# Kernel optimization log

Measured on AMD Instinct MI355X. Metric: run time of the kernel, lower is better.

The kernel has to match this reference:

```python
import jax, jax.numpy as jnp
import numpy as np

B, T, N, D, H = 16, 12, 325, 64, 4
E = 2600
NEG_SLOPE = 0.2
LN_EPS = 1e-5
SM_EPS = 1e-16


def setup_inputs() -> dict:
    key = jax.random.key(0)
    ks = jax.random.split(key, 8)
    x = jax.random.normal(ks[0], (B, T, N, D), dtype=jnp.float32)
    edge_index = jax.random.randint(ks[1], (2, E), 0, N, dtype=jnp.int64)
    W = jax.random.normal(ks[2], (D, H, D), dtype=jnp.float32) * 0.05   # lin weight, [in, heads, out]
    att_src = jax.random.normal(ks[3], (H, D), dtype=jnp.float32) * 0.05
    att_dst = jax.random.normal(ks[4], (H, D), dtype=jnp.float32) * 0.05
    bias = jnp.zeros((D,), dtype=jnp.float32)
    gamma = jnp.ones((D,), dtype=jnp.float32)
    beta = jnp.zeros((D,), dtype=jnp.float32)
    return {"x": x, "W": W, "att_src": att_src, "att_dst": att_dst,
            "bias": bias, "gamma": gamma, "beta": beta, "edge_index": edge_index}


def reference(x, W, att_src, att_dst, bias, gamma, beta, edge_index):
    b, t, n, d = x.shape
    bt = b * t
    xb = x.reshape(bt, n, d)

    # add self-loops (GATConv default add_self_loops=True)
    loops = jnp.arange(n, dtype=edge_index.dtype)
    src = jnp.concatenate([edge_index[0], loops])  # message source j
    dst = jnp.concatenate([edge_index[1], loops])  # message target i

    # per-head linear projection, node axis leading for segment ops: [N, BT, H, D]
    xp = jnp.einsum('bnd,dhf->nbhf', xb, W)

    a_src = jnp.einsum('nbhf,hf->nbh', xp, att_src)  # [N, BT, H]
    a_dst = jnp.einsum('nbhf,hf->nbh', xp, att_dst)

    alpha = a_src[src] + a_dst[dst]                  # [Etot, BT, H]
    alpha = jnp.where(alpha >= 0, alpha, NEG_SLOPE * alpha)

    # segment softmax over incoming edges of each dst node
    m = jax.ops.segment_max(alpha, dst, num_segments=n)        # [N, BT, H]
    e = jnp.exp(alpha - m[dst])
    s = jax.ops.segment_sum(e, dst, num_segments=n)            # [N, BT, H]
    coef = e / (s[dst] + SM_EPS)                               # [Etot, BT, H]

    # weighted scatter-sum aggregation
    msgs = coef[..., None] * xp[src]                           # [Etot, BT, H, D]
    out = jax.ops.segment_sum(msgs, dst, num_segments=n)       # [N, BT, H, D]

    out = out.mean(axis=2) + bias                              # concat=False -> head mean; [N, BT, D]
    out = out.transpose(1, 0, 2).reshape(b, t, n, d)

    # residual + LayerNorm
    y = x + out
    mu = y.mean(axis=-1, keepdims=True)
    var = y.var(axis=-1, keepdims=True)
    return (y - mu) * jax.lax.rsqrt(var + LN_EPS) * gamma + beta
```

## Files before the change

kernel.cpp:

```cpp
#include <hip/hip_runtime.h>

#define Nn 325
#define Dd 64
#define Hh 4
#define Ee 2600
#define BT 192
#define ETOT (Ee+Nn)
#define NROWS (BT*Nn)
#define XPS 136

#define XP_B   (Nn * XPS * 2)
#define COEF_B (ETOT * 8)
#define SMEM_BYTES (XP_B + COEF_B + 2600 + 2600 + ((Nn + 1) * 4) + (ETOT * 4))

typedef __attribute__((ext_vector_type(8))) short bf16x8;
typedef __attribute__((ext_vector_type(4))) float f32x4;

static __device__ __forceinline__ short f2bf(float f) {
    union { float f; unsigned u; } v; v.f = f;
    unsigned r = v.u + 0x7fffu + ((v.u >> 16) & 1u);
    return (short)(r >> 16);
}
static __device__ __forceinline__ float bf_lo(unsigned p) {
    union { unsigned u; float f; } v; v.u = p << 16; return v.f;
}
static __device__ __forceinline__ float bf_hi(unsigned p) {
    union { unsigned u; float f; } v; v.u = p & 0xffff0000u; return v.f;
}

__global__ __launch_bounds__(256) void k_pre(
    const float* __restrict__ W, unsigned short* __restrict__ Wt,
    const int* __restrict__ ei, int* __restrict__ offs, int* __restrict__ elist)
{
    const int t = threadIdx.x;
    if (blockIdx.x < 64) {
        const int f = blockIdx.x * 256 + t;
        const int thr = f >> 6, idx = f & 63;
        const int ct = idx >> 4, kk = (idx >> 3) & 1, j = idx & 7;
        const int w = thr >> 6, lane = thr & 63;
        const int q = lane >> 4, l16 = lane & 15;
        Wt[f] = (unsigned short)f2bf(
            W[(size_t)(kk * 32 + q * 8 + j) * 256 + w * 64 + ct * 16 + l16]);
        return;
    }
    __shared__ int cnt[Nn + 1];
    __shared__ int cur[Nn];
    const int lane = t & 63;
    for (int i = t; i <= Nn; i += 256) cnt[i] = 0;
    __syncthreads();
    for (int e = t; e < ETOT; e += 256) {
        int d = (e < Ee) ? ei[Ee + e] : (e - Ee);
        atomicAdd(&cnt[d + 1], 1);
    }
    __syncthreads();
    if (t < 64) {
        int run = 0;
        for (int c = 0; c < 6; ++c) {
            int i = c * 64 + lane;
            int v = (i <= Nn) ? cnt[i] : 0;
            #pragma unroll
            for (int off = 1; off < 64; off <<= 1) {
                int u = __shfl_up(v, off);
                if (lane >= off) v += u;
            }
            v += run;
            if (i <= Nn) cnt[i] = v;
            run = __shfl(v, 63);
        }
    }
    __syncthreads();
    for (int i = t; i <= Nn; i += 256) offs[i] = cnt[i];
    for (int i = t; i < Nn; i += 256) cur[i] = cnt[i];
    __syncthreads();
    for (int e = t; e < ETOT; e += 256) {
        int s, d;
        if (e < Ee) { s = ei[e]; d = ei[Ee + e]; }
        else        { s = e - Ee; d = e - Ee; }
        int slot = atomicAdd(&cur[d], 1);
        elist[slot] = s;
    }
}

__global__ __launch_bounds__(1024, 4) void k_fused(
    const float* __restrict__ x, const unsigned short* __restrict__ Wt,
    const float* __restrict__ att_src, const float* __restrict__ att_dst,
    const int* __restrict__ offs, const int* __restrict__ elist,
    const float* __restrict__ bias, const float* __restrict__ gamma,
    const float* __restrict__ beta, float* __restrict__ out)
{
    const int bt   = blockIdx.x;
    const int t    = threadIdx.x;
    const int wv   = t >> 6;
    const int lane = t & 63;
    const int q    = lane >> 4;
    const int l16  = lane & 15;
    const int btN  = bt * Nn;

    extern __shared__ char smem[];
    unsigned short* xpS   = (unsigned short*)smem;
    float2*         coefS = (float2*)(smem + XP_B);
    float*          asrcS = (float*)(smem + XP_B + COEF_B);
    float*          adstS = asrcS + 2 * Nn;
    int*            offsS = (int*)(adstS + 2 * Nn);
    int*            elistS= offsS + (Nn + 1);

    for (int i = t; i < ETOT; i += 1024) elistS[i] = elist[i];
    for (int i = t; i <= Nn; i += 1024) offsS[i] = offs[i];

    float accO[6][4];
    #pragma unroll
    for (int i = 0; i < 6; ++i)
        accO[i][0] = accO[i][1] = accO[i][2] = accO[i][3] = 0.f;

    const int hh  = wv >> 3;
    const int rtb = wv & 7;

    #pragma unroll 2
    for (int p = 0; p < 2; ++p) {
        const int h = p * 2 + hh;
        bf16x8 bfr[4][2];
        const bf16x8* wtp = (const bf16x8*)(Wt + (size_t)(h * 64 + lane) * 64);
        #pragma unroll
        for (int ct = 0; ct < 4; ++ct) {
            bfr[ct][0] = wtp[ct * 2];
            bfr[ct][1] = wtp[ct * 2 + 1];
        }
        float avs[4], avd[4];
        #pragma unroll
        for (int ct = 0; ct < 4; ++ct) {
            avs[ct] = att_src[h * 64 + ct * 16 + l16];
            avd[ct] = att_dst[h * 64 + ct * 16 + l16];
        }
        if (p) __syncthreads();

        #pragma unroll
        for (int k3 = 0; k3 < 3; ++k3) {
            const int rt = rtb + 8 * k3;
            if (rt > 20) break;
            bf16x8 afr[2];
            const int na = min(rt * 16 + l16, Nn - 1);
            const float* xr = x + (size_t)(btN + na) * 64 + q * 8;
            #pragma unroll
            for (int kk = 0; kk < 2; ++kk) {
                float4 v0 = *(const float4*)(xr + kk * 32);
                float4 v1 = *(const float4*)(xr + kk * 32 + 4);
                afr[kk][0]=f2bf(v0.x); afr[kk][1]=f2bf(v0.y);
                afr[kk][2]=f2bf(v0.z); afr[kk][3]=f2bf(v0.w);
                afr[kk][4]=f2bf(v1.x); afr[kk][5]=f2bf(v1.y);
                afr[kk][6]=f2bf(v1.z); afr[kk][7]=f2bf(v1.w);
            }
            f32x4 acc[4];
            #pragma unroll
            for (int ct = 0; ct < 4; ++ct) {
                acc[ct] = (f32x4){0.f, 0.f, 0.f, 0.f};
                acc[ct] = __builtin_amdgcn_mfma_f32_16x16x32_bf16(afr[0], bfr[ct][0], acc[ct], 0, 0, 0);
                acc[ct] = __builtin_amdgcn_mfma_f32_16x16x32_bf16(afr[1], bfr[ct][1], acc[ct], 0, 0, 0);
            }
            #pragma unroll
            for (int r = 0; r < 4; ++r) {
                const int n = rt * 16 + q * 4 + r;
                float ps = 0.f, pd = 0.f;
                #pragma unroll
                for (int ct = 0; ct < 4; ++ct) {
                    ps = fmaf(acc[ct][r], avs[ct], ps);
                    pd = fmaf(acc[ct][r], avd[ct], pd);
                }
                #pragma unroll
                for (int off = 1; off <= 8; off <<= 1) {
                    ps += __shfl_xor(ps, off);
                    pd += __shfl_xor(pd, off);
                }
                if (l16 == 0 && n < Nn) {
                    asrcS[n * 2 + hh] = ps;
                    adstS[n * 2 + hh] = pd;
                }
                if (n < Nn) {
                    #pragma unroll
                    for (int ct = 0; ct < 4; ++ct)
                        xpS[n * XPS + (ct * 16 + l16) * 2 + hh] =
                            (unsigned short)f2bf(acc[ct][r]);
                }
            }
        }
        __syncthreads();

        #pragma unroll
        for (int it = 0; it < 6; ++it) {
            const int n = wv * 4 + q + it * 64;
            if (n >= Nn) break;
            const int o0 = offsS[n];
            int deg = offsS[n + 1] - o0;
            deg = min(deg, 48);
            const float adn0 = adstS[n * 2], adn1 = adstS[n * 2 + 1];
            float ex0[3], ex1[3];
            float m0 = -3e38f, m1 = -3e38f;
            #pragma unroll
            for (int r = 0; r < 3; ++r) {
                float a0 = -3e38f, a1 = -3e38f;
                if (r * 16 < deg) {
                    const int e = r * 16 + l16;
                    if (e < deg) {
                        const int j = elistS[o0 + e];
                        const float2 as = *(const float2*)(asrcS + j * 2);
                        a0 = as.x + adn0; a1 = as.y + adn1;
                    }
                }
                a0 = (a0 >= 0.f) ? a0 : 0.2f * a0;
                a1 = (a1 >= 0.f) ? a1 : 0.2f * a1;
                ex0[r] = a0; ex1[r] = a1;
                m0 = fmaxf(m0, a0); m1 = fmaxf(m1, a1);
            }
            #pragma unroll
            for (int off = 1; off <= 8; off <<= 1) {
                m0 = fmaxf(m0, __shfl_xor(m0, off));
                m1 = fmaxf(m1, __shfl_xor(m1, off));
            }
            float s0 = 0.f, s1 = 0.f;
            #pragma unroll
            for (int r = 0; r < 3; ++r) if (r * 16 < deg) {
                ex0[r] = __expf(ex0[r] - m0); s0 += ex0[r];
                ex1[r] = __expf(ex1[r] - m1); s1 += ex1[r];
            }
            #pragma unroll
            for (int off = 1; off <= 8; off <<= 1) {
                s0 += __shfl_xor(s0, off);
                s1 += __shfl_xor(s1, off);
            }
            const float i0 = 1.f / (s0 + 1e-16f);
            const float i1 = 1.f / (s1 + 1e-16f);
            #pragma unroll
            for (int r = 0; r < 3; ++r) if (r * 16 < deg) {
                const int e = r * 16 + l16;
                if (e < deg) coefS[o0 + e] = make_float2(ex0[r] * i0, ex1[r] * i1);
            }

            float f0 = 0.f, f1 = 0.f, f2v = 0.f, f3 = 0.f;
            int e2 = 0;
            for (; e2 + 2 <= deg; e2 += 2) {
                const int ja = elistS[o0 + e2];
                const int jb = elistS[o0 + e2 + 1];
                const float2 ca = coefS[o0 + e2];
                const float2 cb = coefS[o0 + e2 + 1];
                const uint4 ra = *(const uint4*)((const char*)xpS + ja * (XPS * 2) + l16 * 16);
                const uint4 rb = *(const uint4*)((const char*)xpS + jb * (XPS * 2) + l16 * 16);
                f0  = fmaf(ca.x, bf_lo(ra.x), f0);  f0  = fmaf(ca.y, bf_hi(ra.x), f0);
                f1  = fmaf(ca.x, bf_lo(ra.y), f1);  f1  = fmaf(ca.y, bf_hi(ra.y), f1);
                f2v = fmaf(ca.x, bf_lo(ra.z), f2v); f2v = fmaf(ca.y, bf_hi(ra.z), f2v);
                f3  = fmaf(ca.x, bf_lo(ra.w), f3);  f3  = fmaf(ca.y, bf_hi(ra.w), f3);
                f0  = fmaf(cb.x, bf_lo(rb.x), f0);  f0  = fmaf(cb.y, bf_hi(rb.x), f0);
                f1  = fmaf(cb.x, bf_lo(rb.y), f1);  f1  = fmaf(cb.y, bf_hi(rb.y), f1);
                f2v = fmaf(cb.x, bf_lo(rb.z), f2v); f2v = fmaf(cb.y, bf_hi(rb.z), f2v);
                f3  = fmaf(cb.x, bf_lo(rb.w), f3);  f3  = fmaf(cb.y, bf_hi(rb.w), f3);
            }
            if (e2 < deg) {
                const int ja = elistS[o0 + e2];
                const float2 ca = coefS[o0 + e2];
                const uint4 ra = *(const uint4*)((const char*)xpS + ja * (XPS * 2) + l16 * 16);
                f0  = fmaf(ca.x, bf_lo(ra.x), f0);  f0  = fmaf(ca.y, bf_hi(ra.x), f0);
                f1  = fmaf(ca.x, bf_lo(ra.y), f1);  f1  = fmaf(ca.y, bf_hi(ra.y), f1);
                f2v = fmaf(ca.x, bf_lo(ra.z), f2v); f2v = fmaf(ca.y, bf_hi(ra.z), f2v);
                f3  = fmaf(ca.x, bf_lo(ra.w), f3);  f3  = fmaf(ca.y, bf_hi(ra.w), f3);
            }
            accO[it][0] += f0; accO[it][1] += f1;
            accO[it][2] += f2v; accO[it][3] += f3;
        }
    }

    const int f4 = l16 * 4;
    const float4 ga = *(const float4*)(gamma + f4);
    const float4 be = *(const float4*)(beta + f4);
    const float4 bi = *(const float4*)(bias + f4);
    #pragma unroll
    for (int it = 0; it < 6; ++it) {
        const int n = wv * 4 + q + it * 64;
        if (n >= Nn) break;
        const float4 xv = *(const float4*)(x + (size_t)(btN + n) * 64 + f4);
        const float y0 = xv.x + accO[it][0] * 0.25f + bi.x;
        const float y1 = xv.y + accO[it][1] * 0.25f + bi.y;
        const float y2 = xv.z + accO[it][2] * 0.25f + bi.z;
        const float y3 = xv.w + accO[it][3] * 0.25f + bi.w;
        float s1 = y0 + y1 + y2 + y3;
        float s2 = y0*y0 + y1*y1 + y2*y2 + y3*y3;
        #pragma unroll
        for (int off = 1; off <= 8; off <<= 1) {
            s1 += __shfl_xor(s1, off);
            s2 += __shfl_xor(s2, off);
        }
        const float mu  = s1 * (1.f / 64.f);
        const float var = s2 * (1.f / 64.f) - mu * mu;
        const float rr  = rsqrtf(var + 1e-5f);
        float4 o;
        o.x = (y0 - mu) * rr * ga.x + be.x;
        o.y = (y1 - mu) * rr * ga.y + be.y;
        o.z = (y2 - mu) * rr * ga.z + be.z;
        o.w = (y3 - mu) * rr * ga.w + be.w;
        *(float4*)(out + (size_t)(btN + n) * 64 + f4) = o;
    }
}

extern "C" void kernel_launch(void* const* d_in, const int* in_sizes, int n_in,
                              void* d_out, int out_size, void* d_ws, size_t ws_size,
                              hipStream_t stream)
{
    const float* x       = (const float*)d_in[0];
    const float* W       = (const float*)d_in[1];
    const float* att_src = (const float*)d_in[2];
    const float* att_dst = (const float*)d_in[3];
    const float* bias    = (const float*)d_in[4];
    const float* gamma   = (const float*)d_in[5];
    const float* beta    = (const float*)d_in[6];
    const int*   ei      = (const int*)d_in[7];

    unsigned short* Wt = (unsigned short*)d_ws;
    int* offs  = (int*)(Wt + 16384);
    int* elist = offs + (Nn + 1);
    float* out = (float*)d_out;

    hipFuncSetAttribute((const void*)k_fused,
                        hipFuncAttributeMaxDynamicSharedMemorySize, SMEM_BYTES);

    hipLaunchKernelGGL(k_pre, dim3(65), dim3(256), 0, stream,
                       W, Wt, ei, offs, elist);
    hipLaunchKernelGGL(k_fused, dim3(BT), dim3(1024), SMEM_BYTES, stream,
                       x, Wt, att_src, att_dst, offs, elist,
                       bias, gamma, beta, out);
}
```

Before: 139.4 us.

## Pre-convert x to bf16, sort nodes by degree, unroll gather by four

Adds a pre-pass in k_pre that converts all of x to bf16 in workspace, so the fused kernel loads MFMA A fragments directly without per-element conversion. Builds a degree-sorted node permutation (descending degree histogram scan) so that each wave's four node groups have similar in-degree, which reduces divergence in the softmax and aggregation loops. The aggregation inner loop is unrolled to four edges for more LDS load-level parallelism. In exchange, the pre-pass writes and the fused kernel rereads an extra bf16 copy of x, and the output rows written per wave become scattered.

```diff
diff --git a/kernel.cpp b/kernel.cpp
--- a/kernel.cpp
+++ b/kernel.cpp
@@ -11,7 +11,7 @@
 
 #define XP_B   (Nn * XPS * 2)
 #define COEF_B (ETOT * 8)
-#define SMEM_BYTES (XP_B + COEF_B + 2600 + 2600 + ((Nn + 1) * 4) + (ETOT * 4))
+#define SMEM_BYTES (XP_B + COEF_B + 2600 + 2600 + ((Nn + 1) * 4) + (ETOT * 4) + (Nn * 4))
 
 typedef __attribute__((ext_vector_type(8))) short bf16x8;
 typedef __attribute__((ext_vector_type(4))) float f32x4;
@@ -30,7 +30,9 @@
 
 __global__ __launch_bounds__(256) void k_pre(
     const float* __restrict__ W, unsigned short* __restrict__ Wt,
-    const int* __restrict__ ei, int* __restrict__ offs, int* __restrict__ elist)
+    const int* __restrict__ ei, int* __restrict__ offs, int* __restrict__ elist,
+    int* __restrict__ perm, const float* __restrict__ x,
+    unsigned short* __restrict__ xbf)
 {
     const int t = threadIdx.x;
     if (blockIdx.x < 64) {
@@ -43,10 +45,30 @@
             W[(size_t)(kk * 32 + q * 8 + j) * 256 + w * 64 + ct * 16 + l16]);
         return;
     }
+    if (blockIdx.x >= 65) {
+        const int bx = blockIdx.x - 65;
+        #pragma unroll
+        for (int k = 0; k < 8; ++k) {
+            const int idx = bx * 2048 + k * 256 + t;
+            if (idx < (NROWS * Dd) / 4) {
+                float4 v = ((const float4*)x)[idx];
+                ushort4 o;
+                o.x = (unsigned short)f2bf(v.x);
+                o.y = (unsigned short)f2bf(v.y);
+                o.z = (unsigned short)f2bf(v.z);
+                o.w = (unsigned short)f2bf(v.w);
+                ((ushort4*)xbf)[idx] = o;
+            }
+        }
+        return;
+    }
     __shared__ int cnt[Nn + 1];
     __shared__ int cur[Nn];
+    __shared__ int dh[64];
+    __shared__ int startS[64];
     const int lane = t & 63;
     for (int i = t; i <= Nn; i += 256) cnt[i] = 0;
+    if (t < 64) dh[t] = 0;
     __syncthreads();
     for (int e = t; e < ETOT; e += 256) {
         int d = (e < Ee) ? ei[Ee + e] : (e - Ee);
@@ -71,6 +93,19 @@
     __syncthreads();
     for (int i = t; i <= Nn; i += 256) offs[i] = cnt[i];
     for (int i = t; i < Nn; i += 256) cur[i] = cnt[i];
+    for (int n = t; n < Nn; n += 256)
+        atomicAdd(&dh[min(cnt[n + 1] - cnt[n], 63)], 1);
+    __syncthreads();
+    if (t < 64) {
+        int v = dh[63 - lane];
+        int inc = v;
+        #pragma unroll
+        for (int off = 1; off < 64; off <<= 1) {
+            int u = __shfl_up(inc, off);
+            if (lane >= off) inc += u;
+        }
+        startS[63 - lane] = inc - v;
+    }
     __syncthreads();
     for (int e = t; e < ETOT; e += 256) {
         int s, d;
@@ -79,12 +114,18 @@
         int slot = atomicAdd(&cur[d], 1);
         elist[slot] = s;
     }
+    for (int n = t; n < Nn; n += 256) {
+        int slot = atomicAdd(&startS[min(cnt[n + 1] - cnt[n], 63)], 1);
+        perm[slot] = n;
+    }
 }
 
 __global__ __launch_bounds__(1024, 4) void k_fused(
-    const float* __restrict__ x, const unsigned short* __restrict__ Wt,
+    const float* __restrict__ x, const unsigned short* __restrict__ xbf,
+    const unsigned short* __restrict__ Wt,
     const float* __restrict__ att_src, const float* __restrict__ att_dst,
     const int* __restrict__ offs, const int* __restrict__ elist,
+    const int* __restrict__ perm,
     const float* __restrict__ bias, const float* __restrict__ gamma,
     const float* __restrict__ beta, float* __restrict__ out)
 {
@@ -103,9 +144,11 @@
     float*          adstS = asrcS + 2 * Nn;
     int*            offsS = (int*)(adstS + 2 * Nn);
     int*            elistS= offsS + (Nn + 1);
+    int*            permS = elistS + ETOT;
 
     for (int i = t; i < ETOT; i += 1024) elistS[i] = elist[i];
     for (int i = t; i <= Nn; i += 1024) offsS[i] = offs[i];
+    for (int i = t; i < Nn; i += 1024) permS[i] = perm[i];
 
     float accO[6][4];
     #pragma unroll
@@ -114,6 +157,7 @@
 
     const int hh  = wv >> 3;
     const int rtb = wv & 7;
+    const int g   = wv * 4 + q;
 
     #pragma unroll 2
     for (int p = 0; p < 2; ++p) {
@@ -137,18 +181,11 @@
         for (int k3 = 0; k3 < 3; ++k3) {
             const int rt = rtb + 8 * k3;
             if (rt > 20) break;
+            const int na = min(rt * 16 + l16, Nn - 1);
             bf16x8 afr[2];
-            const int na = min(rt * 16 + l16, Nn - 1);
-            const float* xr = x + (size_t)(btN + na) * 64 + q * 8;
-            #pragma unroll
-            for (int kk = 0; kk < 2; ++kk) {
-                float4 v0 = *(const float4*)(xr + kk * 32);
-                float4 v1 = *(const float4*)(xr + kk * 32 + 4);
-                afr[kk][0]=f2bf(v0.x); afr[kk][1]=f2bf(v0.y);
-                afr[kk][2]=f2bf(v0.z); afr[kk][3]=f2bf(v0.w);
-                afr[kk][4]=f2bf(v1.x); afr[kk][5]=f2bf(v1.y);
-                afr[kk][6]=f2bf(v1.z); afr[kk][7]=f2bf(v1.w);
-            }
+            #pragma unroll
+            for (int kk = 0; kk < 2; ++kk)
+                afr[kk] = *(const bf16x8*)(xbf + (size_t)(btN + na) * 64 + kk * 32 + q * 8);
             f32x4 acc[4];
             #pragma unroll
             for (int ct = 0; ct < 4; ++ct) {
@@ -186,8 +223,9 @@
 
         #pragma unroll
         for (int it = 0; it < 6; ++it) {
-            const int n = wv * 4 + q + it * 64;
-            if (n >= Nn) break;
+            const int rk = it * 64 + g;
+            if (rk >= Nn) continue;
+            const int n = permS[rk];
             const int o0 = offsS[n];
             int deg = offsS[n + 1] - o0;
             deg = min(deg, 48);
@@ -236,23 +274,33 @@
 
             float f0 = 0.f, f1 = 0.f, f2v = 0.f, f3 = 0.f;
             int e2 = 0;
-            for (; e2 + 2 <= deg; e2 += 2) {
-                const int ja = elistS[o0 + e2];
-                const int jb = elistS[o0 + e2 + 1];
-                const float2 ca = coefS[o0 + e2];
-                const float2 cb = coefS[o0 + e2 + 1];
-                const uint4 ra = *(const uint4*)((const char*)xpS + ja * (XPS * 2) + l16 * 16);
-                const uint4 rb = *(const uint4*)((const char*)xpS + jb * (XPS * 2) + l16 * 16);
-                f0  = fmaf(ca.x, bf_lo(ra.x), f0);  f0  = fmaf(ca.y, bf_hi(ra.x), f0);
-                f1  = fmaf(ca.x, bf_lo(ra.y), f1);  f1  = fmaf(ca.y, bf_hi(ra.y), f1);
-                f2v = fmaf(ca.x, bf_lo(ra.z), f2v); f2v = fmaf(ca.y, bf_hi(ra.z), f2v);
-                f3  = fmaf(ca.x, bf_lo(ra.w), f3);  f3  = fmaf(ca.y, bf_hi(ra.w), f3);
-                f0  = fmaf(cb.x, bf_lo(rb.x), f0);  f0  = fmaf(cb.y, bf_hi(rb.x), f0);
-                f1  = fmaf(cb.x, bf_lo(rb.y), f1);  f1  = fmaf(cb.y, bf_hi(rb.y), f1);
-                f2v = fmaf(cb.x, bf_lo(rb.z), f2v); f2v = fmaf(cb.y, bf_hi(rb.z), f2v);
-                f3  = fmaf(cb.x, bf_lo(rb.w), f3);  f3  = fmaf(cb.y, bf_hi(rb.w), f3);
-            }
-            if (e2 < deg) {
+            for (; e2 + 4 <= deg; e2 += 4) {
+                const int j0 = elistS[o0 + e2],     j1 = elistS[o0 + e2 + 1];
+                const int j2 = elistS[o0 + e2 + 2], j3 = elistS[o0 + e2 + 3];
+                const float2 c0 = coefS[o0 + e2],     c1 = coefS[o0 + e2 + 1];
+                const float2 c2 = coefS[o0 + e2 + 2], c3 = coefS[o0 + e2 + 3];
+                const uint4 r0 = *(const uint4*)((const char*)xpS + j0 * (XPS * 2) + l16 * 16);
+                const uint4 r1 = *(const uint4*)((const char*)xpS + j1 * (XPS * 2) + l16 * 16);
+                const uint4 r2 = *(const uint4*)((const char*)xpS + j2 * (XPS * 2) + l16 * 16);
+                const uint4 r3 = *(const uint4*)((const char*)xpS + j3 * (XPS * 2) + l16 * 16);
+                f0  = fmaf(c0.x, bf_lo(r0.x), f0);  f0  = fmaf(c0.y, bf_hi(r0.x), f0);
+                f1  = fmaf(c0.x, bf_lo(r0.y), f1);  f1  = fmaf(c0.y, bf_hi(r0.y), f1);
+                f2v = fmaf(c0.x, bf_lo(r0.z), f2v); f2v = fmaf(c0.y, bf_hi(r0.z), f2v);
+                f3  = fmaf(c0.x, bf_lo(r0.w), f3);  f3  = fmaf(c0.y, bf_hi(r0.w), f3);
+                f0  = fmaf(c1.x, bf_lo(r1.x), f0);  f0  = fmaf(c1.y, bf_hi(r1.x), f0);
+                f1  = fmaf(c1.x, bf_lo(r1.y), f1);  f1  = fmaf(c1.y, bf_hi(r1.y), f1);
+                f2v = fmaf(c1.x, bf_lo(r1.z), f2v); f2v = fmaf(c1.y, bf_hi(r1.z), f2v);
+                f3  = fmaf(c1.x, bf_lo(r1.w), f3);  f3  = fmaf(c1.y, bf_hi(r1.w), f3);
+                f0  = fmaf(c2.x, bf_lo(r2.x), f0);  f0  = fmaf(c2.y, bf_hi(r2.x), f0);
+                f1  = fmaf(c2.x, bf_lo(r2.y), f1);  f1  = fmaf(c2.y, bf_hi(r2.y), f1);
+                f2v = fmaf(c2.x, bf_lo(r2.z), f2v); f2v = fmaf(c2.y, bf_hi(r2.z), f2v);
+                f3  = fmaf(c2.x, bf_lo(r2.w), f3);  f3  = fmaf(c2.y, bf_hi(r2.w), f3);
+                f0  = fmaf(c3.x, bf_lo(r3.x), f0);  f0  = fmaf(c3.y, bf_hi(r3.x), f0);
+                f1  = fmaf(c3.x, bf_lo(r3.y), f1);  f1  = fmaf(c3.y, bf_hi(r3.y), f1);
+                f2v = fmaf(c3.x, bf_lo(r3.z), f2v); f2v = fmaf(c3.y, bf_hi(r3.z), f2v);
+                f3  = fmaf(c3.x, bf_lo(r3.w), f3);  f3  = fmaf(c3.y, bf_hi(r3.w), f3);
+            }
+            for (; e2 < deg; ++e2) {
                 const int ja = elistS[o0 + e2];
                 const float2 ca = coefS[o0 + e2];
                 const uint4 ra = *(const uint4*)((const char*)xpS + ja * (XPS * 2) + l16 * 16);
@@ -272,8 +320,9 @@
     const float4 bi = *(const float4*)(bias + f4);
     #pragma unroll
     for (int it = 0; it < 6; ++it) {
-        const int n = wv * 4 + q + it * 64;
-        if (n >= Nn) break;
+        const int rk = it * 64 + g;
+        if (rk >= Nn) continue;
+        const int n = permS[rk];
         const float4 xv = *(const float4*)(x + (size_t)(btN + n) * 64 + f4);
         const float y0 = xv.x + accO[it][0] * 0.25f + bi.x;
         const float y1 = xv.y + accO[it][1] * 0.25f + bi.y;
@@ -311,17 +360,19 @@
     const float* beta    = (const float*)d_in[6];
     const int*   ei      = (const int*)d_in[7];
 
-    unsigned short* Wt = (unsigned short*)d_ws;
-    int* offs  = (int*)(Wt + 16384);
+    unsigned short* Wt  = (unsigned short*)d_ws;
+    unsigned short* xbf = Wt + 16384;
+    int* offs  = (int*)(xbf + (size_t)NROWS * Dd);
     int* elist = offs + (Nn + 1);
+    int* perm  = elist + ETOT;
     float* out = (float*)d_out;
 
     hipFuncSetAttribute((const void*)k_fused,
                         hipFuncAttributeMaxDynamicSharedMemorySize, SMEM_BYTES);
 
-    hipLaunchKernelGGL(k_pre, dim3(65), dim3(256), 0, stream,
-                       W, Wt, ei, offs, elist);
+    hipLaunchKernelGGL(k_pre, dim3(65 + 488), dim3(256), 0, stream,
+                       W, Wt, ei, offs, elist, perm, x, xbf);
     hipLaunchKernelGGL(k_fused, dim3(BT), dim3(1024), SMEM_BYTES, stream,
-                       x, Wt, att_src, att_dst, offs, elist,
+                       x, xbf, Wt, att_src, att_dst, offs, elist, perm,
                        bias, gamma, beta, out);
 }
```

After: 134.2 us. -3.8%, faster.
